# Kernel optimization log

Hardware: AMD Instinct MI355X
Metric: run time of the kernel (lower is better)

Reference implementation:

```python
import jax, jax.numpy as jnp
import numpy as np

T, G, K, N = 131072, 64, 1024, 512  # batch_sum, batch_count, k, n
M_MAX = 4096  # static upper bound on any group size (setup guarantees <= 3072)
PAD = 128     # tile alignment for padded offsets


def setup_inputs() -> dict:
    key = jax.random.key(0)
    k1, k2 = jax.random.split(key)
    a = jax.random.normal(k1, (T, K), dtype=jnp.float32)
    b = jax.random.normal(k2, (G, K, N), dtype=jnp.float32) / np.float32(np.sqrt(K))
    rng = np.random.default_rng(0)
    d = rng.integers(-1024, 1024, G // 2)
    deltas = np.concatenate([d, -d])
    rng.shuffle(deltas)
    sizes = (T // G) + deltas  # each in [1024, 3072], sums exactly to T
    offsets = np.concatenate([[0], np.cumsum(sizes)[:-1]])
    padded = ((sizes + PAD - 1) // PAD) * PAD
    padded_offsets = np.concatenate([[0], np.cumsum(padded)[:-1]])
    return {
        "a": a,
        "b": b,
        "batch_sizes": jnp.asarray(sizes, dtype=jnp.int32),
        "batch_offsets": jnp.asarray(offsets, dtype=jnp.int32),
        "batch_padded_offsets": jnp.asarray(padded_offsets, dtype=jnp.int32),
    }


def reference(a, b, batch_sizes, batch_offsets, batch_padded_offsets):
    # Grouped GEMM: for each group g, out[off_g : off_g+size_g] = a[rows] @ b[g].
    # jit-friendly: scan over groups with a fixed M_MAX window, mask invalid rows.
    T_, _ = a.shape
    n_out = b.shape[-1]
    iota = jnp.arange(M_MAX)

    def body(out, xs):
        off, size, bg = xs
        rows = jnp.clip(off + iota, 0, T_ - 1)          # [M_MAX]
        mask = iota < size                               # [M_MAX]
        a_g = jnp.where(mask[:, None], a[rows], 0.0)     # [M_MAX, K]
        y = a_g @ bg                                     # [M_MAX, N]
        out = out.at[rows].add(y)                        # masked rows add zeros
        return out, None

    out0 = jnp.zeros((T_, n_out), dtype=a.dtype)
    out, _ = jax.lax.scan(body, out0, (batch_offsets, batch_sizes, b))
    return out
```

## Files before the change

### kernel.cpp

```cpp
#include <hip/hip_runtime.h>
#include <hip/hip_bf16.h>
#include <stdint.h>

#define T_ROWS 131072
#define GCNT   64
#define KDIM   1024
#define NDIM   512
#define BM     256
#define BN     256
#define BK     64
#define KTILES (KDIM / BK)
#define MT_MAX 640
#define NBLK   (MT_MAX * 2)

typedef __attribute__((ext_vector_type(4))) float f32x4;
typedef __attribute__((ext_vector_type(8))) short s16x8;
typedef __attribute__((ext_vector_type(4))) short s16x4;
typedef __attribute__((address_space(3))) unsigned int lds_u32;
typedef const __attribute__((address_space(1))) unsigned int gbl_u32;

static __device__ __forceinline__ short f2bf(float f) {
  __hip_bfloat16 h = __float2bfloat16(f);
  return __builtin_bit_cast(short, h);
}

__global__ __launch_bounds__(256) void bt_kernel(const float* __restrict__ b,
                                                 char* __restrict__ bt) {
  __shared__ short lt[64 * 130];
  int bid = blockIdx.x;
  int kt = bid & 15, nt = (bid >> 4) & 3, g = bid >> 6;
  int t = threadIdx.x;
  const float* src = b + ((size_t)(g * KDIM + kt * BK)) * NDIM + nt * 128;
#pragma unroll
  for (int i = 0; i < 32; i++) {
    int idx = i * 256 + t;
    int kk = idx >> 7, nn = idx & 127;
    lt[kk * 130 + nn] = f2bf(src[(size_t)kk * NDIM + nn]);
  }
  __syncthreads();
  char* dst = bt + ((size_t)bid << 14);
#pragma unroll
  for (int j = 0; j < 4; j++) {
    int chunk = j * 256 + t;
    int n = chunk >> 3;
    int slot = (chunk & 7) ^ (n & 7);
    s16x8 v;
#pragma unroll
    for (int i = 0; i < 8; i++) v[i] = lt[(slot * 8 + i) * 130 + n];
    *(s16x8*)(dst + (size_t)chunk * 16) = v;
  }
}

__global__ __launch_bounds__(512, 2) void gemm8(
    const float* __restrict__ a, const char* __restrict__ bt,
    const int* __restrict__ sizes, const int* __restrict__ offs,
    float* __restrict__ out) {
  __shared__ __align__(16) short lds_a[2][BM * BK];
  __shared__ __align__(16) char lds_b[2][BN * BK * 2];

  int bid0 = blockIdx.x;
  int bid = (bid0 & 7) * (NBLK / 8) + (bid0 >> 3);
  int bn = bid & 1;
  int tm = bid >> 1;

  int g = -1, m_loc = 0, base = 0;
#pragma unroll
  for (int i = 0; i < GCNT; i++) {
    int ps = (sizes[i] + 127) & ~127;
    int tg = (ps + 255) >> 8;
    if (tm >= base && tm < base + tg) { g = i; m_loc = (tm - base) << 8; }
    base += tg;
  }
  if (g < 0) return;
  int size = sizes[g], off = offs[g], valid = size - m_loc;

  int t = threadIdx.x, lane = t & 63, wid = t >> 6;
  int wm = wid >> 2, wn = wid & 3, lr = lane & 15, q = lane >> 4;

  int r0 = t >> 4, c16 = t & 15;
  int aoff[8];
#pragma unroll
  for (int i = 0; i < 8; i++) {
    int row = off + m_loc + i * 32 + r0;
    if (row >= T_ROWS) row = T_ROWS - 1;
    aoff[i] = row * KDIM + c16 * 4;
  }
  int a_wbyte = r0 * 128 + (((c16 >> 1) ^ (r0 & 7)) << 4) + (c16 & 1) * 8;

  const char* btbase = bt + ((size_t)g << 20);

  f32x4 acc[8][4];
#pragma unroll
  for (int i = 0; i < 8; i++)
#pragma unroll
    for (int j = 0; j < 4; j++) acc[i][j] = (f32x4){0.f, 0.f, 0.f, 0.f};
  f32x4 va[8];
  s16x8 af[4], bf0[4], bf1[4];

  auto issueA = [&](int kt, int h) {
#pragma unroll
    for (int i = 0; i < 4; i++)
      va[h * 4 + i] = *(const f32x4*)(a + aoff[h * 4 + i] + kt * BK);
  };
  auto issueB = [&](int kt, int c, int h) {
#pragma unroll
    for (int i = 0; i < 2; i++) {
      int wc = wid * 4 + h * 2 + i;
      int sub = wc >> 4;
      int cc = (wc & 15) * 64 + lane;
      const char* gsrc =
          btbase + (((size_t)((bn * 2 + sub) * 16 + kt)) << 14) + cc * 16;
      __builtin_amdgcn_global_load_lds(
          (gbl_u32*)gsrc, (lds_u32*)((char*)lds_b[c] + wc * 1024), 16, 0, 0);
    }
  };
  auto writeA = [&](int c) {
    char* db = (char*)lds_a[c] + a_wbyte;
#pragma unroll
    for (int i = 0; i < 8; i++) {
      s16x4 v;
#pragma unroll
      for (int e = 0; e < 4; e++) v[e] = f2bf(va[i][e]);
      *(s16x4*)(db + i * 4096) = v;
    }
  };
  auto dsA = [&](int c, int half, int ks) {
#pragma unroll
    for (int i = 0; i < 4; i++) {
      int row = wm * 128 + (half * 4 + i) * 16 + lr;
      int slot = (ks * 4 + q) ^ (row & 7);
      af[i] = *(const s16x8*)((const char*)lds_a[c] + row * 128 + slot * 16);
    }
  };
  auto dsB = [&](int c, int ks, s16x8* bf) {
#pragma unroll
    for (int fn = 0; fn < 4; fn++) {
      int n = wn * 64 + fn * 16 + lr;
      int slot = (ks * 4 + q) ^ (n & 7);
      bf[fn] = *(const s16x8*)((const char*)lds_b[c] + (n >> 7) * 16384 +
                               (n & 127) * 128 + slot * 16);
    }
  };
  auto bar = [&]() {
    __builtin_amdgcn_s_barrier();
    __builtin_amdgcn_sched_barrier(0);
  };
  auto mfmaQ = [&](const s16x8* bf, int fmb) {
    __builtin_amdgcn_s_setprio(1);
#pragma unroll
    for (int fm = 0; fm < 4; fm++)
#pragma unroll
      for (int fn = 0; fn < 4; fn++)
        acc[fmb + fm][fn] = __builtin_amdgcn_mfma_f32_16x16x32_bf16(
            af[fm], bf[fn], acc[fmb + fm][fn], 0, 0, 0);
    __builtin_amdgcn_s_setprio(0);
  };

  issueA(0, 0);
  issueA(0, 1);
  issueB(0, 0, 0);
  issueB(0, 0, 1);
  writeA(0);
  asm volatile("s_waitcnt vmcnt(0) lgkmcnt(0)" ::: "memory");
  bar();

  for (int kt = 0; kt < KTILES; kt++) {
    int cur = kt & 1, nxt = cur ^ 1;
    bool more = (kt + 1 < KTILES);
    dsA(cur, 0, 0);
    dsB(cur, 0, bf0);
    if (more) issueA(kt + 1, 0);
    bar();
    mfmaQ(bf0, 0);
    bar();
    dsA(cur, 0, 1);
    dsB(cur, 1, bf1);
    if (more) issueA(kt + 1, 1);
    bar();
    mfmaQ(bf1, 0);
    bar();
    dsA(cur, 1, 0);
    if (more) issueB(kt + 1, nxt, 0);
    bar();
    mfmaQ(bf0, 4);
    bar();
    dsA(cur, 1, 1);
    if (more) issueB(kt + 1, nxt, 1);
    bar();
    mfmaQ(bf1, 4);
    bar();
    if (more) {
      writeA(nxt);
      asm volatile("s_waitcnt vmcnt(0) lgkmcnt(0)" ::: "memory");
      bar();
    }
  }

  size_t orow0 = (size_t)(off + m_loc);
#pragma unroll
  for (int fm = 0; fm < 8; fm++) {
#pragma unroll
    for (int j = 0; j < 4; j++) {
      int rm = wm * 128 + fm * 16 + q * 4 + j;
      if (rm < valid) {
        float* orow = out + (orow0 + rm) * NDIM + bn * BN + wn * 64 + lr;
#pragma unroll
        for (int fn = 0; fn < 4; fn++) orow[fn * 16] = acc[fm][fn][j];
      }
    }
  }
}

__global__ __launch_bounds__(512, 2) void gemm_fb(
    const float* __restrict__ a, const float* __restrict__ b,
    const int* __restrict__ sizes, const int* __restrict__ offs,
    float* __restrict__ out) {
  __shared__ __align__(16) short lds_a[2][BM * BK];
  __shared__ __align__(16) char lds_b[2][BN * BK * 2];

  int bid0 = blockIdx.x;
  int bid = (bid0 & 7) * (NBLK / 8) + (bid0 >> 3);
  int bn = bid & 1;
  int tm = bid >> 1;

  int g = -1, m_loc = 0, base = 0;
#pragma unroll
  for (int i = 0; i < GCNT; i++) {
    int ps = (sizes[i] + 127) & ~127;
    int tg = (ps + 255) >> 8;
    if (tm >= base && tm < base + tg) { g = i; m_loc = (tm - base) << 8; }
    base += tg;
  }
  if (g < 0) return;
  int size = sizes[g], off = offs[g], valid = size - m_loc;

  int t = threadIdx.x, lane = t & 63, wid = t >> 6;
  int wm = wid >> 2, wn = wid & 3, lr = lane & 15, q = lane >> 4;

  int r0 = t >> 4, c16 = t & 15;
  int aoff[8];
#pragma unroll
  for (int i = 0; i < 8; i++) {
    int row = off + m_loc + i * 32 + r0;
    if (row >= T_ROWS) row = T_ROWS - 1;
    aoff[i] = row * KDIM + c16 * 4;
  }
  int a_wbyte = r0 * 128 + (((c16 >> 1) ^ (r0 & 7)) << 4) + (c16 & 1) * 8;
  int fb_n = t >> 1, fb_kh = (t & 1) * 32;

  f32x4 acc[8][4];
#pragma unroll
  for (int i = 0; i < 8; i++)
#pragma unroll
    for (int j = 0; j < 4; j++) acc[i][j] = (f32x4){0.f, 0.f, 0.f, 0.f};
  f32x4 va[8];

  auto loadA = [&](int kt) {
#pragma unroll
    for (int i = 0; i < 8; i++) va[i] = *(const f32x4*)(a + aoff[i] + kt * BK);
  };
  auto writeA = [&](int c) {
    char* db = (char*)lds_a[c] + a_wbyte;
#pragma unroll
    for (int i = 0; i < 8; i++) {
      s16x4 v;
#pragma unroll
      for (int e = 0; e < 4; e++) v[e] = f2bf(va[i][e]);
      *(s16x4*)(db + i * 4096) = v;
    }
  };
  auto stageB = [&](int kt, int c) {
    const float* p = b + (size_t)g * KDIM * NDIM +
                     (size_t)(kt * BK + fb_kh) * NDIM + bn * BN + fb_n;
    float vals[32];
#pragma unroll
    for (int i = 0; i < 32; i++) vals[i] = p[(size_t)i * NDIM];
    int nn = fb_n & 127;
    char* lb = (char*)lds_b[c] + (fb_n >> 7) * 16384 + nn * 128;
#pragma unroll
    for (int i8 = 0; i8 < 4; i8++) {
      int slot = (fb_kh >> 3) + i8;
      s16x8 v;
#pragma unroll
      for (int e = 0; e < 8; e++) v[e] = f2bf(vals[i8 * 8 + e]);
      *(s16x8*)(lb + (((slot ^ (nn & 7))) << 4)) = v;
    }
  };
  auto compute = [&](int c) {
#pragma unroll
    for (int ks = 0; ks < 2; ks++) {
      s16x8 af[8], bfr[4];
#pragma unroll
      for (int fm = 0; fm < 8; fm++) {
        int row = wm * 128 + fm * 16 + lr;
        int slot = (ks * 4 + q) ^ (row & 7);
        af[fm] = *(const s16x8*)((const char*)lds_a[c] + row * 128 + slot * 16);
      }
#pragma unroll
      for (int fn = 0; fn < 4; fn++) {
        int n = wn * 64 + fn * 16 + lr;
        int slot = (ks * 4 + q) ^ (n & 7);
        bfr[fn] = *(const s16x8*)((const char*)lds_b[c] + (n >> 7) * 16384 +
                                  (n & 127) * 128 + slot * 16);
      }
#pragma unroll
      for (int fm = 0; fm < 8; fm++)
#pragma unroll
        for (int fn = 0; fn < 4; fn++)
          acc[fm][fn] = __builtin_amdgcn_mfma_f32_16x16x32_bf16(
              af[fm], bfr[fn], acc[fm][fn], 0, 0, 0);
    }
  };

  loadA(0);
  stageB(0, 0);
  writeA(0);
  __syncthreads();
  int cur = 0;
  for (int kt = 0; kt < KTILES; kt++) {
    if (kt + 1 < KTILES) loadA(kt + 1);
    compute(cur);
    if (kt + 1 < KTILES) {
      stageB(kt + 1, cur ^ 1);
      writeA(cur ^ 1);
      __syncthreads();
      cur ^= 1;
    }
  }
  size_t orow0 = (size_t)(off + m_loc);
#pragma unroll
  for (int fm = 0; fm < 8; fm++) {
#pragma unroll
    for (int j = 0; j < 4; j++) {
      int rm = wm * 128 + fm * 16 + q * 4 + j;
      if (rm < valid) {
        float* orow = out + (orow0 + rm) * NDIM + bn * BN + wn * 64 + lr;
#pragma unroll
        for (int fn = 0; fn < 4; fn++) orow[fn * 16] = acc[fm][fn][j];
      }
    }
  }
}

extern "C" void kernel_launch(void* const* d_in, const int* in_sizes, int n_in,
                              void* d_out, int out_size, void* d_ws,
                              size_t ws_size, hipStream_t stream) {
  const float* a = (const float*)d_in[0];
  const float* b = (const float*)d_in[1];
  const int* sizes = (const int*)d_in[2];
  const int* offs = (const int*)d_in[3];
  float* out = (float*)d_out;

  const size_t bt_bytes = (size_t)GCNT * KDIM * NDIM * 2;
  if (ws_size >= bt_bytes) {
    bt_kernel<<<GCNT * 64, 256, 0, stream>>>(b, (char*)d_ws);
    gemm8<<<NBLK, 512, 0, stream>>>(a, (const char*)d_ws, sizes, offs, out);
  } else {
    gemm_fb<<<NBLK, 512, 0, stream>>>(a, b, sizes, offs, out);
  }
}
```

Before: 307.5 us.

## Prefetch A two k-tiles ahead and split bf16 conversion from LDS write

New measurement: 375.6 us. +22.1%, slower.

```diff
diff --git a/kernel.cpp b/kernel.cpp
--- a/kernel.cpp
+++ b/kernel.cpp
@@ -95,12 +95,27 @@
 #pragma unroll
     for (int j = 0; j < 4; j++) acc[i][j] = (f32x4){0.f, 0.f, 0.f, 0.f};
   f32x4 va[8];
+  s16x4 pk[8];
   s16x8 af[4], bf0[4], bf1[4];
 
   auto issueA = [&](int kt, int h) {
 #pragma unroll
     for (int i = 0; i < 4; i++)
       va[h * 4 + i] = *(const f32x4*)(a + aoff[h * 4 + i] + kt * BK);
+  };
+  auto cvtHalf = [&](int h) {
+#pragma unroll
+    for (int i = 0; i < 4; i++) {
+      s16x4 v;
+#pragma unroll
+      for (int e = 0; e < 4; e++) v[e] = f2bf(va[h * 4 + i][e]);
+      pk[h * 4 + i] = v;
+    }
+  };
+  auto writeA = [&](int c) {
+    char* db = (char*)lds_a[c] + a_wbyte;
+#pragma unroll
+    for (int i = 0; i < 8; i++) *(s16x4*)(db + i * 4096) = pk[i];
   };
   auto issueB = [&](int kt, int c, int h) {
 #pragma unroll
@@ -114,16 +129,6 @@
           (gbl_u32*)gsrc, (lds_u32*)((char*)lds_b[c] + wc * 1024), 16, 0, 0);
     }
   };
-  auto writeA = [&](int c) {
-    char* db = (char*)lds_a[c] + a_wbyte;
-#pragma unroll
-    for (int i = 0; i < 8; i++) {
-      s16x4 v;
-#pragma unroll
-      for (int e = 0; e < 4; e++) v[e] = f2bf(va[i][e]);
-      *(s16x4*)(db + i * 4096) = v;
-    }
-  };
   auto dsA = [&](int c, int half, int ks) {
 #pragma unroll
     for (int i = 0; i < 4; i++) {
@@ -158,40 +163,52 @@
 
   issueA(0, 0);
   issueA(0, 1);
+  cvtHalf(0);
+  cvtHalf(1);
+  writeA(0);
   issueB(0, 0, 0);
   issueB(0, 0, 1);
-  writeA(0);
-  asm volatile("s_waitcnt vmcnt(0) lgkmcnt(0)" ::: "memory");
+  issueA(1, 0);
+  issueA(1, 1);
+  asm volatile("s_waitcnt vmcnt(8) lgkmcnt(0)" ::: "memory");
+  __builtin_amdgcn_sched_barrier(0);
   bar();
 
   for (int kt = 0; kt < KTILES; kt++) {
     int cur = kt & 1, nxt = cur ^ 1;
-    bool more = (kt + 1 < KTILES);
+    bool moreB = (kt + 1 < KTILES);
+    bool moreA = (kt + 2 < KTILES);
     dsA(cur, 0, 0);
     dsB(cur, 0, bf0);
-    if (more) issueA(kt + 1, 0);
+    if (moreB) issueB(kt + 1, nxt, 0);
     bar();
     mfmaQ(bf0, 0);
     bar();
     dsA(cur, 0, 1);
     dsB(cur, 1, bf1);
-    if (more) issueA(kt + 1, 1);
+    if (moreB) issueB(kt + 1, nxt, 1);
     bar();
     mfmaQ(bf1, 0);
     bar();
     dsA(cur, 1, 0);
-    if (more) issueB(kt + 1, nxt, 0);
+    if (moreB) cvtHalf(0);
+    if (moreA) issueA(kt + 2, 0);
     bar();
     mfmaQ(bf0, 4);
     bar();
     dsA(cur, 1, 1);
-    if (more) issueB(kt + 1, nxt, 1);
+    if (moreB) cvtHalf(1);
+    if (moreA) issueA(kt + 2, 1);
     bar();
     mfmaQ(bf1, 4);
     bar();
-    if (more) {
+    if (moreB) {
       writeA(nxt);
-      asm volatile("s_waitcnt vmcnt(0) lgkmcnt(0)" ::: "memory");
+      if (moreA)
+        asm volatile("s_waitcnt vmcnt(8) lgkmcnt(0)" ::: "memory");
+      else
+        asm volatile("s_waitcnt vmcnt(0) lgkmcnt(0)" ::: "memory");
+      __builtin_amdgcn_sched_barrier(0);
       bar();
     }
   }
```

## Shrink GEMM tiles to 128x128 with 4 waves and simpler double-buffered loop

Applied to the files above, without the earlier changes.

After: 426.3 us. 1.39x slower.

```diff
diff --git a/kernel.cpp b/kernel.cpp
--- a/kernel.cpp
+++ b/kernel.cpp
@@ -6,12 +6,12 @@
 #define GCNT   64
 #define KDIM   1024
 #define NDIM   512
-#define BM     256
-#define BN     256
+#define BM     128
+#define BN     128
 #define BK     64
 #define KTILES (KDIM / BK)
-#define MT_MAX 640
-#define NBLK   (MT_MAX * 2)
+#define MT_MAX 1088
+#define NBLK   (MT_MAX * 4)
 
 typedef __attribute__((ext_vector_type(4))) float f32x4;
 typedef __attribute__((ext_vector_type(8))) short s16x8;
@@ -51,7 +51,7 @@
   }
 }
 
-__global__ __launch_bounds__(512, 2) void gemm8(
+__global__ __launch_bounds__(256, 2) void gemm2(
     const float* __restrict__ a, const char* __restrict__ bt,
     const int* __restrict__ sizes, const int* __restrict__ offs,
     float* __restrict__ out) {
@@ -60,148 +60,116 @@
 
   int bid0 = blockIdx.x;
   int bid = (bid0 & 7) * (NBLK / 8) + (bid0 >> 3);
-  int bn = bid & 1;
-  int tm = bid >> 1;
+  int bn = bid & 3;
+  int tm = bid >> 2;
 
   int g = -1, m_loc = 0, base = 0;
 #pragma unroll
   for (int i = 0; i < GCNT; i++) {
-    int ps = (sizes[i] + 127) & ~127;
-    int tg = (ps + 255) >> 8;
-    if (tm >= base && tm < base + tg) { g = i; m_loc = (tm - base) << 8; }
+    int tg = ((sizes[i] + 127) & ~127) >> 7;
+    if (tm >= base && tm < base + tg) { g = i; m_loc = (tm - base) << 7; }
     base += tg;
   }
   if (g < 0) return;
   int size = sizes[g], off = offs[g], valid = size - m_loc;
 
   int t = threadIdx.x, lane = t & 63, wid = t >> 6;
-  int wm = wid >> 2, wn = wid & 3, lr = lane & 15, q = lane >> 4;
+  int wm = wid >> 1, wn = wid & 1, lr = lane & 15, q = lane >> 4;
 
   int r0 = t >> 4, c16 = t & 15;
   int aoff[8];
 #pragma unroll
   for (int i = 0; i < 8; i++) {
-    int row = off + m_loc + i * 32 + r0;
+    int row = off + m_loc + i * 16 + r0;
     if (row >= T_ROWS) row = T_ROWS - 1;
     aoff[i] = row * KDIM + c16 * 4;
   }
   int a_wbyte = r0 * 128 + (((c16 >> 1) ^ (r0 & 7)) << 4) + (c16 & 1) * 8;
 
-  const char* btbase = bt + ((size_t)g << 20);
-
-  f32x4 acc[8][4];
-#pragma unroll
-  for (int i = 0; i < 8; i++)
+  const char* btimg = bt + ((size_t)((g << 6) + (bn << 4)) << 14);
+
+  f32x4 acc[4][4];
+#pragma unroll
+  for (int i = 0; i < 4; i++)
 #pragma unroll
     for (int j = 0; j < 4; j++) acc[i][j] = (f32x4){0.f, 0.f, 0.f, 0.f};
   f32x4 va[8];
-  s16x8 af[4], bf0[4], bf1[4];
-
-  auto issueA = [&](int kt, int h) {
-#pragma unroll
-    for (int i = 0; i < 4; i++)
-      va[h * 4 + i] = *(const f32x4*)(a + aoff[h * 4 + i] + kt * BK);
-  };
-  auto issueB = [&](int kt, int c, int h) {
-#pragma unroll
-    for (int i = 0; i < 2; i++) {
-      int wc = wid * 4 + h * 2 + i;
-      int sub = wc >> 4;
-      int cc = (wc & 15) * 64 + lane;
-      const char* gsrc =
-          btbase + (((size_t)((bn * 2 + sub) * 16 + kt)) << 14) + cc * 16;
+
+  auto loadA = [&](int kt) {
+#pragma unroll
+    for (int i = 0; i < 8; i++)
+      va[i] = *(const f32x4*)(a + aoff[i] + kt * BK);
+  };
+  auto writeA = [&](int c) {
+    char* db = (char*)lds_a[c] + a_wbyte;
+#pragma unroll
+    for (int i = 0; i < 8; i++) {
+      s16x4 v;
+#pragma unroll
+      for (int e = 0; e < 4; e++) v[e] = f2bf(va[i][e]);
+      *(s16x4*)(db + i * 2048) = v;
+    }
+  };
+  auto stageB = [&](int kt, int c) {
+#pragma unroll
+    for (int i = 0; i < 4; i++) {
+      int wc = wid * 4 + i;
+      int cc = wc * 64 + lane;
+      const char* gsrc = btimg + ((size_t)kt << 14) + (size_t)cc * 16;
       __builtin_amdgcn_global_load_lds(
           (gbl_u32*)gsrc, (lds_u32*)((char*)lds_b[c] + wc * 1024), 16, 0, 0);
     }
   };
-  auto writeA = [&](int c) {
-    char* db = (char*)lds_a[c] + a_wbyte;
-#pragma unroll
-    for (int i = 0; i < 8; i++) {
-      s16x4 v;
-#pragma unroll
-      for (int e = 0; e < 4; e++) v[e] = f2bf(va[i][e]);
-      *(s16x4*)(db + i * 4096) = v;
-    }
-  };
-  auto dsA = [&](int c, int half, int ks) {
-#pragma unroll
-    for (int i = 0; i < 4; i++) {
-      int row = wm * 128 + (half * 4 + i) * 16 + lr;
-      int slot = (ks * 4 + q) ^ (row & 7);
-      af[i] = *(const s16x8*)((const char*)lds_a[c] + row * 128 + slot * 16);
-    }
-  };
-  auto dsB = [&](int c, int ks, s16x8* bf) {
-#pragma unroll
-    for (int fn = 0; fn < 4; fn++) {
-      int n = wn * 64 + fn * 16 + lr;
-      int slot = (ks * 4 + q) ^ (n & 7);
-      bf[fn] = *(const s16x8*)((const char*)lds_b[c] + (n >> 7) * 16384 +
-                               (n & 127) * 128 + slot * 16);
-    }
-  };
-  auto bar = [&]() {
-    __builtin_amdgcn_s_barrier();
-    __builtin_amdgcn_sched_barrier(0);
-  };
-  auto mfmaQ = [&](const s16x8* bf, int fmb) {
-    __builtin_amdgcn_s_setprio(1);
-#pragma unroll
-    for (int fm = 0; fm < 4; fm++)
-#pragma unroll
-      for (int fn = 0; fn < 4; fn++)
-        acc[fmb + fm][fn] = __builtin_amdgcn_mfma_f32_16x16x32_bf16(
-            af[fm], bf[fn], acc[fmb + fm][fn], 0, 0, 0);
-    __builtin_amdgcn_s_setprio(0);
-  };
-
-  issueA(0, 0);
-  issueA(0, 1);
-  issueB(0, 0, 0);
-  issueB(0, 0, 1);
+  auto compute = [&](int c) {
+#pragma unroll
+    for (int ks = 0; ks < 2; ks++) {
+      s16x8 af[4], bf[4];
+#pragma unroll
+      for (int fm = 0; fm < 4; fm++) {
+        int row = wm * 64 + fm * 16 + lr;
+        int slot = (ks * 4 + q) ^ (row & 7);
+        af[fm] = *(const s16x8*)((const char*)lds_a[c] + row * 128 + slot * 16);
+      }
+#pragma unroll
+      for (int fn = 0; fn < 4; fn++) {
+        int n = wn * 64 + fn * 16 + lr;
+        int slot = (ks * 4 + q) ^ (n & 7);
+        bf[fn] = *(const s16x8*)((const char*)lds_b[c] + n * 128 + slot * 16);
+      }
+#pragma unroll
+      for (int fm = 0; fm < 4; fm++)
+#pragma unroll
+        for (int fn = 0; fn < 4; fn++)
+          acc[fm][fn] = __builtin_amdgcn_mfma_f32_16x16x32_bf16(
+              af[fm], bf[fn], acc[fm][fn], 0, 0, 0);
+    }
+  };
+
+  loadA(0);
+  stageB(0, 0);
   writeA(0);
-  asm volatile("s_waitcnt vmcnt(0) lgkmcnt(0)" ::: "memory");
-  bar();
+  __syncthreads();
 
   for (int kt = 0; kt < KTILES; kt++) {
     int cur = kt & 1, nxt = cur ^ 1;
     bool more = (kt + 1 < KTILES);
-    dsA(cur, 0, 0);
-    dsB(cur, 0, bf0);
-    if (more) issueA(kt + 1, 0);
-    bar();
-    mfmaQ(bf0, 0);
-    bar();
-    dsA(cur, 0, 1);
-    dsB(cur, 1, bf1);
-    if (more) issueA(kt + 1, 1);
-    bar();
-    mfmaQ(bf1, 0);
-    bar();
-    dsA(cur, 1, 0);
-    if (more) issueB(kt + 1, nxt, 0);
-    bar();
-    mfmaQ(bf0, 4);
-    bar();
-    dsA(cur, 1, 1);
-    if (more) issueB(kt + 1, nxt, 1);
-    bar();
-    mfmaQ(bf1, 4);
-    bar();
+    if (more) {
+      loadA(kt + 1);
+      stageB(kt + 1, nxt);
+    }
+    compute(cur);
     if (more) {
       writeA(nxt);
-      asm volatile("s_waitcnt vmcnt(0) lgkmcnt(0)" ::: "memory");
-      bar();
+      __syncthreads();
     }
   }
 
   size_t orow0 = (size_t)(off + m_loc);
 #pragma unroll
-  for (int fm = 0; fm < 8; fm++) {
+  for (int fm = 0; fm < 4; fm++) {
 #pragma unroll
     for (int j = 0; j < 4; j++) {
-      int rm = wm * 128 + fm * 16 + q * 4 + j;
+      int rm = wm * 64 + fm * 16 + q * 4 + j;
       if (rm < valid) {
         float* orow = out + (orow0 + rm) * NDIM + bn * BN + wn * 64 + lr;
 #pragma unroll
@@ -211,7 +179,7 @@
   }
 }
 
-__global__ __launch_bounds__(512, 2) void gemm_fb(
+__global__ __launch_bounds__(256, 2) void gemm_fb(
     const float* __restrict__ a, const float* __restrict__ b,
     const int* __restrict__ sizes, const int* __restrict__ offs,
     float* __restrict__ out) {
@@ -220,37 +188,36 @@
 
   int bid0 = blockIdx.x;
   int bid = (bid0 & 7) * (NBLK / 8) + (bid0 >> 3);
-  int bn = bid & 1;
-  int tm = bid >> 1;
+  int bn = bid & 3;
+  int tm = bid >> 2;
 
   int g = -1, m_loc = 0, base = 0;
 #pragma unroll
   for (int i = 0; i < GCNT; i++) {
-    int ps = (sizes[i] + 127) & ~127;
-    int tg = (ps + 255) >> 8;
-    if (tm >= base && tm < base + tg) { g = i; m_loc = (tm - base) << 8; }
+    int tg = ((sizes[i] + 127) & ~127) >> 7;
+    if (tm >= base && tm < base + tg) { g = i; m_loc = (tm - base) << 7; }
     base += tg;
   }
   if (g < 0) return;
   int size = sizes[g], off = offs[g], valid = size - m_loc;
 
   int t = threadIdx.x, lane = t & 63, wid = t >> 6;
-  int wm = wid >> 2, wn = wid & 3, lr = lane & 15, q = lane >> 4;
+  int wm = wid >> 1, wn = wid & 1, lr = lane & 15, q = lane >> 4;
 
   int r0 = t >> 4, c16 = t & 15;
   int aoff[8];
 #pragma unroll
   for (int i = 0; i < 8; i++) {
-    int row = off + m_loc + i * 32 + r0;
+    int row = off + m_loc + i * 16 + r0;
     if (row >= T_ROWS) row = T_ROWS - 1;
     aoff[i] = row * KDIM + c16 * 4;
   }
   int a_wbyte = r0 * 128 + (((c16 >> 1) ^ (r0 & 7)) << 4) + (c16 & 1) * 8;
   int fb_n = t >> 1, fb_kh = (t & 1) * 32;
 
-  f32x4 acc[8][4];
-#pragma unroll
-  for (int i = 0; i < 8; i++)
+  f32x4 acc[4][4];
+#pragma unroll
+  for (int i = 0; i < 4; i++)
 #pragma unroll
     for (int j = 0; j < 4; j++) acc[i][j] = (f32x4){0.f, 0.f, 0.f, 0.f};
   f32x4 va[8];
@@ -266,7 +233,7 @@
       s16x4 v;
 #pragma unroll
       for (int e = 0; e < 4; e++) v[e] = f2bf(va[i][e]);
-      *(s16x4*)(db + i * 4096) = v;
+      *(s16x4*)(db + i * 2048) = v;
     }
   };
   auto stageB = [&](int kt, int c) {
@@ -275,24 +242,23 @@
     float vals[32];
 #pragma unroll
     for (int i = 0; i < 32; i++) vals[i] = p[(size_t)i * NDIM];
-    int nn = fb_n & 127;
-    char* lb = (char*)lds_b[c] + (fb_n >> 7) * 16384 + nn * 128;
+    char* lb = (char*)lds_b[c] + fb_n * 128;
 #pragma unroll
     for (int i8 = 0; i8 < 4; i8++) {
       int slot = (fb_kh >> 3) + i8;
       s16x8 v;
 #pragma unroll
       for (int e = 0; e < 8; e++) v[e] = f2bf(vals[i8 * 8 + e]);
-      *(s16x8*)(lb + (((slot ^ (nn & 7))) << 4)) = v;
+      *(s16x8*)(lb + ((slot ^ (fb_n & 7)) << 4)) = v;
     }
   };
   auto compute = [&](int c) {
 #pragma unroll
     for (int ks = 0; ks < 2; ks++) {
-      s16x8 af[8], bfr[4];
-#pragma unroll
-      for (int fm = 0; fm < 8; fm++) {
-        int row = wm * 128 + fm * 16 + lr;
+      s16x8 af[4], bf[4];
+#pragma unroll
+      for (int fm = 0; fm < 4; fm++) {
+        int row = wm * 64 + fm * 16 + lr;
         int slot = (ks * 4 + q) ^ (row & 7);
         af[fm] = *(const s16x8*)((const char*)lds_a[c] + row * 128 + slot * 16);
       }
@@ -300,15 +266,14 @@
       for (int fn = 0; fn < 4; fn++) {
         int n = wn * 64 + fn * 16 + lr;
         int slot = (ks * 4 + q) ^ (n & 7);
-        bfr[fn] = *(const s16x8*)((const char*)lds_b[c] + (n >> 7) * 16384 +
-                                  (n & 127) * 128 + slot * 16);
-      }
-#pragma unroll
-      for (int fm = 0; fm < 8; fm++)
+        bf[fn] = *(const s16x8*)((const char*)lds_b[c] + n * 128 + slot * 16);
+      }
+#pragma unroll
+      for (int fm = 0; fm < 4; fm++)
 #pragma unroll
         for (int fn = 0; fn < 4; fn++)
           acc[fm][fn] = __builtin_amdgcn_mfma_f32_16x16x32_bf16(
-              af[fm], bfr[fn], acc[fm][fn], 0, 0, 0);
+              af[fm], bf[fn], acc[fm][fn], 0, 0, 0);
     }
   };
 
@@ -316,23 +281,23 @@
   stageB(0, 0);
   writeA(0);
   __syncthreads();
-  int cur = 0;
   for (int kt = 0; kt < KTILES; kt++) {
-    if (kt + 1 < KTILES) loadA(kt + 1);
+    int cur = kt & 1, nxt = cur ^ 1;
+    bool more = (kt + 1 < KTILES);
+    if (more) loadA(kt + 1);
     compute(cur);
-    if (kt + 1 < KTILES) {
-      stageB(kt + 1, cur ^ 1);
-      writeA(cur ^ 1);
+    if (more) {
+      stageB(kt + 1, nxt);
+      writeA(nxt);
       __syncthreads();
-      cur ^= 1;
     }
   }
   size_t orow0 = (size_t)(off + m_loc);
 #pragma unroll
-  for (int fm = 0; fm < 8; fm++) {
+  for (int fm = 0; fm < 4; fm++) {
 #pragma unroll
     for (int j = 0; j < 4; j++) {
-      int rm = wm * 128 + fm * 16 + q * 4 + j;
+      int rm = wm * 64 + fm * 16 + q * 4 + j;
       if (rm < valid) {
         float* orow = out + (orow0 + rm) * NDIM + bn * BN + wn * 64 + lr;
 #pragma unroll
@@ -354,8 +319,8 @@
   const size_t bt_bytes = (size_t)GCNT * KDIM * NDIM * 2;
   if (ws_size >= bt_bytes) {
     bt_kernel<<<GCNT * 64, 256, 0, stream>>>(b, (char*)d_ws);
-    gemm8<<<NBLK, 512, 0, stream>>>(a, (const char*)d_ws, sizes, offs, out);
+    gemm2<<<NBLK, 256, 0, stream>>>(a, (const char*)d_ws, sizes, offs, out);
   } else {
-    gemm_fb<<<NBLK, 512, 0, stream>>>(a, b, sizes, offs, out);
-  }
-}
+    gemm_fb<<<NBLK, 256, 0, stream>>>(a, b, sizes, offs, out);
+  }
+}
```

## Prefetch B tiles two stages ahead and relax waitcnt in grouped GEMM mainloop

Applied to the files above, without the earlier changes.

After: 351.3 us. 14.2% more time.

```diff
diff --git a/kernel.cpp b/kernel.cpp
--- a/kernel.cpp
+++ b/kernel.cpp
@@ -102,6 +102,16 @@
     for (int i = 0; i < 4; i++)
       va[h * 4 + i] = *(const f32x4*)(a + aoff[h * 4 + i] + kt * BK);
   };
+  auto writeA = [&](int c) {
+    char* db = (char*)lds_a[c] + a_wbyte;
+#pragma unroll
+    for (int i = 0; i < 8; i++) {
+      s16x4 v;
+#pragma unroll
+      for (int e = 0; e < 4; e++) v[e] = f2bf(va[i][e]);
+      *(s16x4*)(db + i * 4096) = v;
+    }
+  };
   auto issueB = [&](int kt, int c, int h) {
 #pragma unroll
     for (int i = 0; i < 2; i++) {
@@ -114,16 +124,6 @@
           (gbl_u32*)gsrc, (lds_u32*)((char*)lds_b[c] + wc * 1024), 16, 0, 0);
     }
   };
-  auto writeA = [&](int c) {
-    char* db = (char*)lds_a[c] + a_wbyte;
-#pragma unroll
-    for (int i = 0; i < 8; i++) {
-      s16x4 v;
-#pragma unroll
-      for (int e = 0; e < 4; e++) v[e] = f2bf(va[i][e]);
-      *(s16x4*)(db + i * 4096) = v;
-    }
-  };
   auto dsA = [&](int c, int half, int ks) {
 #pragma unroll
     for (int i = 0; i < 4; i++) {
@@ -141,9 +141,9 @@
                                (n & 127) * 128 + slot * 16);
     }
   };
-  auto bar = [&]() {
-    __builtin_amdgcn_s_barrier();
+  auto pbar = [&]() {
     __builtin_amdgcn_sched_barrier(0);
+    __builtin_amdgcn_s_barrier();
   };
   auto mfmaQ = [&](const s16x8* bf, int fmb) {
     __builtin_amdgcn_s_setprio(1);
@@ -154,46 +154,70 @@
         acc[fmb + fm][fn] = __builtin_amdgcn_mfma_f32_16x16x32_bf16(
             af[fm], bf[fn], acc[fmb + fm][fn], 0, 0, 0);
     __builtin_amdgcn_s_setprio(0);
+    __builtin_amdgcn_sched_barrier(0);
   };
 
   issueA(0, 0);
   issueA(0, 1);
+  writeA(0);
   issueB(0, 0, 0);
   issueB(0, 0, 1);
-  writeA(0);
-  asm volatile("s_waitcnt vmcnt(0) lgkmcnt(0)" ::: "memory");
-  bar();
-
-  for (int kt = 0; kt < KTILES; kt++) {
+  issueB(1, 1, 0);
+  issueB(1, 1, 1);
+  asm volatile("s_waitcnt vmcnt(4) lgkmcnt(0)" ::: "memory");
+  __builtin_amdgcn_sched_barrier(0);
+  __builtin_amdgcn_s_barrier();
+
+  for (int kt = 0; kt < KTILES - 2; kt++) {
     int cur = kt & 1, nxt = cur ^ 1;
-    bool more = (kt + 1 < KTILES);
     dsA(cur, 0, 0);
     dsB(cur, 0, bf0);
-    if (more) issueA(kt + 1, 0);
-    bar();
+    issueA(kt + 1, 0);
+    pbar();
     mfmaQ(bf0, 0);
-    bar();
+    __builtin_amdgcn_s_barrier();
     dsA(cur, 0, 1);
     dsB(cur, 1, bf1);
-    if (more) issueA(kt + 1, 1);
-    bar();
+    issueA(kt + 1, 1);
+    pbar();
     mfmaQ(bf1, 0);
-    bar();
+    __builtin_amdgcn_s_barrier();
     dsA(cur, 1, 0);
-    if (more) issueB(kt + 1, nxt, 0);
-    bar();
+    issueB(kt + 2, cur, 0);
+    pbar();
     mfmaQ(bf0, 4);
-    bar();
+    __builtin_amdgcn_s_barrier();
     dsA(cur, 1, 1);
-    if (more) issueB(kt + 1, nxt, 1);
-    bar();
+    issueB(kt + 2, cur, 1);
+    pbar();
     mfmaQ(bf1, 4);
-    bar();
-    if (more) {
-      writeA(nxt);
-      asm volatile("s_waitcnt vmcnt(0) lgkmcnt(0)" ::: "memory");
-      bar();
-    }
+    __builtin_amdgcn_s_barrier();
+    writeA(nxt);
+    asm volatile("s_waitcnt lgkmcnt(0)" ::: "memory");
+    __builtin_amdgcn_sched_barrier(0);
+    __builtin_amdgcn_s_barrier();
+  }
+
+  {
+    dsA(0, 0, 0); dsB(0, 0, bf0); issueA(15, 0);
+    pbar(); mfmaQ(bf0, 0); __builtin_amdgcn_s_barrier();
+    dsA(0, 0, 1); dsB(0, 1, bf1); issueA(15, 1);
+    pbar(); mfmaQ(bf1, 0); __builtin_amdgcn_s_barrier();
+    dsA(0, 1, 0); pbar(); mfmaQ(bf0, 4); __builtin_amdgcn_s_barrier();
+    dsA(0, 1, 1); pbar(); mfmaQ(bf1, 4); __builtin_amdgcn_s_barrier();
+    writeA(1);
+    asm volatile("s_waitcnt lgkmcnt(0)" ::: "memory");
+    __builtin_amdgcn_sched_barrier(0);
+    __builtin_amdgcn_s_barrier();
+  }
+  {
+    dsA(1, 0, 0); dsB(1, 0, bf0); pbar(); mfmaQ(bf0, 0);
+    __builtin_amdgcn_s_barrier();
+    dsA(1, 0, 1); dsB(1, 1, bf1); pbar(); mfmaQ(bf1, 0);
+    __builtin_amdgcn_s_barrier();
+    dsA(1, 1, 0); pbar(); mfmaQ(bf0, 4);
+    __builtin_amdgcn_s_barrier();
+    dsA(1, 1, 1); pbar(); mfmaQ(bf1, 4);
   }
 
   size_t orow0 = (size_t)(off + m_loc);
```
